# Performance work log

Measured on AMD Instinct MI355X. Metric: run time of the kernel, lower is better.

## Reference

```python
import jax, jax.numpy as jnp
import numpy as np

MAX_NODES = 8192
MAX_EDGES = 16384
D = 64
NEG = -1e10


def setup_inputs() -> dict:
    key = jax.random.key(0)
    k1, k2, k3, k4, k5, k6 = jax.random.split(key, 6)
    N, E = MAX_NODES, MAX_EDGES
    nodes = jax.random.normal(k1, (N, D), jnp.float32)
    edges = jax.random.normal(k2, (E, D), jnp.float32)
    receivers = jax.random.randint(k3, (E,), 0, N, jnp.int32)
    senders = jax.random.randint(k4, (E,), 0, N, jnp.int32)
    active_nodes = jnp.ones((N,), jnp.float32)
    active_edges = (jnp.arange(E) < E // 4).astype(jnp.float32)  # prefix of active edges
    Wq = jax.random.normal(k5, (D, D), jnp.float32) / jnp.sqrt(jnp.float32(D))
    Wp = jax.random.normal(k6, (D, 1), jnp.float32) * 0.05
    bq = jnp.zeros((D,), jnp.float32)
    bp = jnp.full((1,), -4.0, jnp.float32)
    return dict(nodes=nodes, edges=edges, receivers=receivers, senders=senders,
                active_nodes=active_nodes, active_edges=active_edges,
                Wq=Wq, bq=bq, Wp=Wp, bp=bp)


def _incr_edges(aedges, n):
    # Closed form of n steps of x <- clip(x @ (I + superdiag), 0, 1):
    # out[j] = 1 iff any(aedges[j-n : j+1]) != 0, then last slot forced to 0.
    c = jnp.cumsum(aedges)
    idx = jnp.arange(aedges.shape[0])
    prev = jnp.where(idx - n - 1 >= 0, c[jnp.clip(idx - n - 1, 0)], 0.0)
    out = ((c - prev) > 0).astype(aedges.dtype)
    return out.at[-1].set(0.0)


def reference(nodes, edges, receivers, senders, active_nodes, active_edges, Wq, bq, Wp, bp):
    N, E = MAX_NODES, MAX_EDGES
    key = jax.random.key(42)
    key_prob, key_edges, key_samp = jax.random.split(key, 3)
    nids = jnp.arange(N)
    e_active = active_edges.sum().astype(jnp.int32)

    # 1-2. edge-generation probability per node + Bernoulli sampling of generators
    probs = jax.nn.sigmoid(nodes @ Wp + bp)[:, 0]                       # [N]
    gens = (jax.random.uniform(key_prob, (N,)) < probs * active_nodes).astype(jnp.float32)

    # 3-4. queries and pairwise cosine-similarity scores[i, j] = cos(q_i, h_j)
    queries = nodes @ Wq + bq                                           # [N, D]
    num = queries @ nodes.T                                             # [N, N]
    qn = jnp.sum(queries * queries, -1)                                 # [N]
    hn = jnp.sum(nodes * nodes, -1)                                     # [N]
    scores = num / (jnp.sqrt(qn[:, None] * hn[None, :]) + 1e-8)
    scores = jnp.clip(scores, -10000.0, 10000.0)
    scores = jnp.where(active_nodes[None, :] > 0, scores, NEG)
    gens = gens * (scores.max(-1) > -jnp.inf).astype(jnp.float32)       # threshold = -inf
    scores = jnp.where(jnp.eye(N, dtype=bool), NEG, scores)             # no self-loops

    # 5. sample target j* per generating node (softmax mode)
    select = jnp.where(gens > 0, jax.random.categorical(key_samp, scores, axis=-1), 0)

    # drop generators whose edge (i, j*) already exists
    is_s = nids[:, None] == senders[None, :]                            # [N, E]
    is_r = select[:, None] == receivers[None, :]                        # [N, E]
    exist = jnp.logical_and(is_s, is_r).any(-1) & (gens > 0)
    gens = jnp.where(exist, 0.0, gens)

    # 6. scatter new edges into the fixed-size buffers
    allowed = E - e_active - 1
    n_gens = jnp.clip(gens.astype(jnp.int32).sum(), 0, allowed)
    naedges = _incr_edges(active_edges, n_gens)
    mask_new = naedges * (1.0 - active_edges)                           # [E]
    new_edges = edges + jax.random.normal(key_edges, edges.shape) * mask_new[:, None]

    t1 = (jnp.cumsum(gens) * gens - 1.0).astype(jnp.int32) + (e_active * gens).astype(jnp.int32)
    nsend = jax.ops.segment_sum(nids, t1, E)
    nsend = jnp.where(mask_new > 0, nsend, senders)

    t2 = jnp.cumsum(gens) * gens - gens
    t2 = jnp.where(gens > 0, t2.astype(jnp.int32), -1) + (e_active * gens).astype(jnp.int32)
    nrec = jax.ops.segment_sum(select, t2, E)
    nrec = jnp.where(mask_new > 0, nrec, receivers)

    nrec = jnp.where(naedges > 0, nrec, N - 1)
    nsend = jnp.where(naedges > 0, nsend, N - 1)
    return new_edges, nsend, nrec, naedges
```

## Files before the change

kernel.cpp:

```cpp
#include <hip/hip_runtime.h>
#include <stdint.h>

#define NN 8192
#define NE 16384
#define DD 64
#define GCAP 512
#define SLICES 32
#define NEGV -1e10f
#define TINYF 1.17549435e-38f
#define SQRT2F 1.41421356237f

__device__ __forceinline__ uint2 tf2x32(uint32_t k0, uint32_t k1, uint32_t x0, uint32_t x1) {
  uint32_t ks2 = k0 ^ k1 ^ 0x1BD11BDAu;
  x0 += k0; x1 += k1;
#define TF_R(r) { x0 += x1; x1 = (x1 << (r)) | (x1 >> (32 - (r))); x1 ^= x0; }
  TF_R(13) TF_R(15) TF_R(26) TF_R(6)
  x0 += k1; x1 += ks2 + 1u;
  TF_R(17) TF_R(29) TF_R(16) TF_R(24)
  x0 += ks2; x1 += k0 + 2u;
  TF_R(13) TF_R(15) TF_R(26) TF_R(6)
  x0 += k0; x1 += k1 + 3u;
  TF_R(17) TF_R(29) TF_R(16) TF_R(24)
  x0 += k1; x1 += ks2 + 4u;
  TF_R(13) TF_R(15) TF_R(26) TF_R(6)
  x0 += ks2; x1 += k0 + 5u;
#undef TF_R
  return make_uint2(x0, x1);
}
__device__ __forceinline__ uint2 jax_subkey(uint32_t i) { return tf2x32(0u, 42u, 0u, i); }
__device__ __forceinline__ uint32_t rbits(uint2 k, uint32_t idx) {
  uint2 r = tf2x32(k.x, k.y, 0u, idx);
  return r.x ^ r.y;
}
__device__ __forceinline__ float u01f(uint32_t b) {
  return __uint_as_float((b >> 9) | 0x3F800000u) - 1.0f;
}
__device__ __forceinline__ float erfinv_xla(float x) {
  float w = -log1pf(-x * x);
  float p;
  if (w < 5.0f) {
    w -= 2.5f;
    p = 2.81022636e-08f;
    p = fmaf(p, w, 3.43273939e-07f);
    p = fmaf(p, w, -3.5233877e-06f);
    p = fmaf(p, w, -4.39150654e-06f);
    p = fmaf(p, w, 0.00021858087f);
    p = fmaf(p, w, -0.00125372503f);
    p = fmaf(p, w, -0.00417768164f);
    p = fmaf(p, w, 0.246640727f);
    p = fmaf(p, w, 1.50140941f);
  } else {
    w = sqrtf(w) - 3.0f;
    p = -0.000200214257f;
    p = fmaf(p, w, 0.000100950558f);
    p = fmaf(p, w, 0.00134934322f);
    p = fmaf(p, w, -0.00367342844f);
    p = fmaf(p, w, 0.00573950773f);
    p = fmaf(p, w, -0.0076224613f);
    p = fmaf(p, w, 0.00943887047f);
    p = fmaf(p, w, 1.00167406f);
    p = fmaf(p, w, 2.83297682f);
  }
  return p * x;
}
__device__ __forceinline__ float jax_normal(uint2 k, uint32_t idx) {
  float f = u01f(rbits(k, idx));
  float lo = __uint_as_float(0xBF7FFFFFu);
  float u = fmaxf(lo, f * 2.0f + lo);
  return SQRT2F * erfinv_xla(u);
}
__device__ __forceinline__ float jax_gumbel(uint2 k, uint32_t idx) {
  float f = u01f(rbits(k, idx));
  float u = fmaxf(TINYF, f + TINYF);
  return -logf(-logf(u));
}


__global__ void sg_gens(const float* __restrict__ nodes, const float* __restrict__ Wp,
                        const float* __restrict__ bp, const float* __restrict__ anodes,
                        int* __restrict__ gens0, float* __restrict__ hn) {
  int lane = threadIdx.x & 63;
  int i = blockIdx.x * 4 + (threadIdx.x >> 6);
  float v = nodes[i * DD + lane];
  float ss = v * v;
  float dp = v * Wp[lane];
  for (int off = 32; off > 0; off >>= 1) {
    ss += __shfl_xor(ss, off, 64);
    dp += __shfl_xor(dp, off, 64);
  }
  if (lane == 0) {
    hn[i] = ss;
    float x = dp + bp[0];
    float p = 1.0f / (1.0f + expf(-x));
    uint2 kp = jax_subkey(0u);
    float u = u01f(rbits(kp, (uint32_t)i));
    gens0[i] = (u < p * anodes[i]) ? 1 : 0;
  }
}

__global__ void sg_scan(const float* __restrict__ aedges, const int* __restrict__ gens0,
                        int* __restrict__ c, int* __restrict__ gidx, int* __restrict__ sc) {
  __shared__ int ts[256];
  int t = threadIdx.x;
  int base = t * 64;
  uint64_t bits = 0;
  int s = 0;
  const float4* a4 = (const float4*)(aedges + base);
  for (int k4 = 0; k4 < 16; k4++) {
    float4 v = a4[k4];
    if (v.x != 0.0f) { bits |= 1ull << (4 * k4 + 0); s++; }
    if (v.y != 0.0f) { bits |= 1ull << (4 * k4 + 1); s++; }
    if (v.z != 0.0f) { bits |= 1ull << (4 * k4 + 2); s++; }
    if (v.w != 0.0f) { bits |= 1ull << (4 * k4 + 3); s++; }
  }
  ts[t] = s;
  __syncthreads();
  for (int off = 1; off < 256; off <<= 1) {
    int add = (t >= off) ? ts[t - off] : 0;
    __syncthreads();
    ts[t] += add;
    __syncthreads();
  }
  int run = ts[t] - s;
  for (int k = 0; k < 64; k++) {
    run += (int)((bits >> k) & 1ull);
    c[base + k] = run;
  }
  if (t == 255) { sc[1] = ts[255]; sc[2] = NE - ts[255] - 1; }
  __syncthreads();
  int b2 = t * 32;
  uint32_t gb = 0;
  int s2 = 0;
  const int4* g4 = (const int4*)(gens0 + b2);
  for (int k4 = 0; k4 < 8; k4++) {
    int4 v = g4[k4];
    if (v.x) { gb |= 1u << (4 * k4 + 0); s2++; }
    if (v.y) { gb |= 1u << (4 * k4 + 1); s2++; }
    if (v.z) { gb |= 1u << (4 * k4 + 2); s2++; }
    if (v.w) { gb |= 1u << (4 * k4 + 3); s2++; }
  }
  ts[t] = s2;
  __syncthreads();
  for (int off = 1; off < 256; off <<= 1) {
    int add = (t >= off) ? ts[t - off] : 0;
    __syncthreads();
    ts[t] += add;
    __syncthreads();
  }
  int r = ts[t] - s2;
  for (int k = 0; k < 32; k++)
    if ((gb >> k) & 1u) gidx[r++] = b2 + k;
  if (t == 255) sc[0] = ts[255];
}

__global__ void sg_query(const float* __restrict__ nodes, const float* __restrict__ Wq,
                         const float* __restrict__ bq, const int* __restrict__ gidx,
                         const int* __restrict__ sc, float* __restrict__ qg,
                         float* __restrict__ qnrm) {
  int g = blockIdx.x;
  int G = min(sc[0], GCAP);
  if (g >= G) return;
  int i = gidx[g];
  int t = threadIdx.x;
  const float* nr = nodes + (size_t)i * DD;
  float acc = bq[t];
  for (int k = 0; k < DD; k++) acc = fmaf(nr[k], Wq[k * DD + t], acc);
  qg[g * DD + t] = acc;
  float ss = acc * acc;
  for (int off = 32; off > 0; off >>= 1) ss += __shfl_xor(ss, off, 64);
  if (t == 0) qnrm[g] = ss;
}

__global__ __launch_bounds__(256) void sg_part(
    const float* __restrict__ nodes, const float* __restrict__ anodes,
    const float* __restrict__ hn, const int* __restrict__ gidx,
    const int* __restrict__ sc, const float* __restrict__ qg,
    const float* __restrict__ qnrm, float* __restrict__ party,
    int* __restrict__ partj) {
  __shared__ float sq[4][DD];
  __shared__ float sqn[4];
  __shared__ int si[4];
  __shared__ float wy[4][4];
  __shared__ int wj[4][4];
  int G = min(sc[0], GCAP);
  int nGq = (G + 3) >> 2;
  int total = nGq * SLICES;
  int t = threadIdx.x;
  int wid = t >> 6, lane = t & 63;
  uint2 ks = jax_subkey(2u);
  for (int item = blockIdx.x; item < total; item += gridDim.x) {
    int gq = item >> 5, s = item & 31;
    int g0 = gq * 4;
    if (t < DD) {
      for (int u = 0; u < 4; u++)
        sq[u][t] = (g0 + u < G) ? qg[(g0 + u) * DD + t] : 0.0f;
    }
    if (t < 4) {
      int g = g0 + t;
      si[t] = (g < G) ? gidx[g] : -1;
      sqn[t] = (g < G) ? qnrm[g] : 1.0f;
    }
    __syncthreads();
    int j = s * 256 + t;
    float4 nv[16];
    const float4* np4 = (const float4*)(nodes + (size_t)j * DD);
    for (int k4 = 0; k4 < 16; k4++) nv[k4] = np4[k4];
    float hnj = hn[j];
    float act = anodes[j];
    float yy[4];
    for (int u = 0; u < 4; u++) {
      int iu = si[u];
      if (iu < 0) { yy[u] = -INFINITY; continue; }
      float num = 0.0f;
      for (int k4 = 0; k4 < 16; k4++) {
        const float4 qv = *(const float4*)&sq[u][4 * k4];
        num += nv[k4].x * qv.x + nv[k4].y * qv.y + nv[k4].z * qv.z + nv[k4].w * qv.w;
      }
      float denom = sqrtf(sqn[u] * hnj) + 1e-8f;
      float sco = num / denom;
      sco = fminf(fmaxf(sco, -10000.0f), 10000.0f);
      if (!(act > 0.0f)) sco = NEGV;
      if (j == iu) sco = NEGV;
      yy[u] = sco + jax_gumbel(ks, (uint32_t)iu * (uint32_t)NN + (uint32_t)j);
    }
    for (int u = 0; u < 4; u++) {
      float y = yy[u];
      int bj = j;
      for (int off = 32; off > 0; off >>= 1) {
        float oy = __shfl_xor(y, off, 64);
        int oj = __shfl_xor(bj, off, 64);
        if (oy > y || (oy == y && oj < bj)) { y = oy; bj = oj; }
      }
      if (lane == 0) { wy[u][wid] = y; wj[u][wid] = bj; }
    }
    __syncthreads();
    if (t < 4) {
      int u = t;
      if (g0 + u < G) {
        float y = wy[u][0];
        int bj = wj[u][0];
        for (int w = 1; w < 4; w++) {
          if (wy[u][w] > y || (wy[u][w] == y && wj[u][w] < bj)) { y = wy[u][w]; bj = wj[u][w]; }
        }
        party[(g0 + u) * SLICES + s] = y;
        partj[(g0 + u) * SLICES + s] = bj;
      }
    }
    __syncthreads();
  }
}

__global__ void sg_reduce(const int* __restrict__ sc, const float* __restrict__ party,
                          const int* __restrict__ partj, int* __restrict__ sel,
                          int* __restrict__ keptf) {
  int g = blockIdx.x;
  int G = min(sc[0], GCAP);
  if (g >= G) return;
  int t = threadIdx.x;
  float y = (t < SLICES) ? party[g * SLICES + t] : -INFINITY;
  int bj = (t < SLICES) ? partj[g * SLICES + t] : 0x7fffffff;
  for (int off = 32; off > 0; off >>= 1) {
    float oy = __shfl_xor(y, off, 64);
    int oj = __shfl_xor(bj, off, 64);
    if (oy > y || (oy == y && oj < bj)) { y = oy; bj = oj; }
  }
  if (t == 0) { sel[g] = bj; keptf[g] = 1; }
}

__global__ void sg_exist2(const int* __restrict__ senders, const int* __restrict__ receivers,
                          const int* __restrict__ gidx, const int* __restrict__ sel,
                          const int* __restrict__ sc, int* __restrict__ keptf) {
  __shared__ int lg[GCAP], ls[GCAP];
  int G = min(sc[0], GCAP);
  int t = threadIdx.x;
  for (int g = t; g < G; g += 256) { lg[g] = gidx[g]; ls[g] = sel[g]; }
  __syncthreads();
  int e = blockIdx.x * 256 + t;
  int se = senders[e], re = receivers[e];
  for (int g = 0; g < G; g++)
    if (se == lg[g] && re == ls[g]) keptf[g] = 0;
}

__global__ void sg_rank(const int* __restrict__ gidx, const int* __restrict__ sel,
                        const int* __restrict__ keptf, int* __restrict__ sc,
                        int* __restrict__ fid, int* __restrict__ fsel) {
  __shared__ int ts[256];
  int t = threadIdx.x;
  int G = min(sc[0], GCAP);
  int base = t * 32;
  int s = 0;
  for (int k = 0; k < 32; k++) { int g = base + k; if (g < G) s += keptf[g]; }
  ts[t] = s;
  __syncthreads();
  for (int off = 1; off < 256; off <<= 1) {
    int add = (t >= off) ? ts[t - off] : 0;
    __syncthreads();
    ts[t] += add;
    __syncthreads();
  }
  int r = ts[t] - s;
  for (int k = 0; k < 32; k++) {
    int g = base + k;
    if (g < G && keptf[g]) { fid[r] = gidx[g]; fsel[r] = sel[g]; r++; }
  }
  if (t == 255) {
    int kt = ts[255];
    int allowed = sc[2];
    int ng = kt > 0 ? kt : 0;
    if (ng > allowed) ng = allowed;
    sc[3] = kt; sc[4] = ng;
  }
}

__global__ void sg_mask(const float* __restrict__ aedges, const int* __restrict__ senders,
                        const int* __restrict__ receivers, const int* __restrict__ c,
                        const int* __restrict__ sc, const int* __restrict__ fid,
                        const int* __restrict__ fsel, float* __restrict__ out_send,
                        float* __restrict__ out_rec, float* __restrict__ out_na) {
  int e = blockIdx.x * 256 + threadIdx.x;
  if (e >= NE) return;
  int n = sc[4], ea = sc[1], kept = sc[3];
  int ce = c[e];
  int pidx = e - n - 1;
  int prev = (pidx >= 0) ? c[pidx] : 0;
  int na = ((ce - prev) > 0) ? 1 : 0;
  if (e == NE - 1) na = 0;
  float a = aedges[e];
  float mv = na ? (1.0f - a) : 0.0f;
  float ns, nr;
  if (!na) {
    ns = nr = (float)(NN - 1);
  } else if (mv > 0.0f) {
    int r = e - ea;
    bool ok = (r >= 0 && r < kept);
    ns = ok ? (float)fid[r] : 0.0f;
    nr = ok ? (float)fsel[r] : 0.0f;
  } else {
    ns = (float)senders[e];
    nr = (float)receivers[e];
  }
  out_send[e] = ns;
  out_rec[e] = nr;
  out_na[e] = (float)na;
}

__global__ void sg_edges(const float* __restrict__ edges, const float* __restrict__ aedges,
                         const int* __restrict__ c, const int* __restrict__ sc,
                         float* __restrict__ out_edges) {
  int t4 = blockIdx.x * 256 + threadIdx.x;
  float4 v = ((const float4*)edges)[t4];
  int e = t4 >> 4;
  int n = sc[4];
  int ce = c[e];
  int pidx = e - n - 1;
  int prev = (pidx >= 0) ? c[pidx] : 0;
  int na = ((ce - prev) > 0 && e != NE - 1) ? 1 : 0;
  float mv = na ? (1.0f - aedges[e]) : 0.0f;
  if (mv != 0.0f) {
    uint2 ke = jax_subkey(1u);
    uint32_t base = (uint32_t)t4 * 4u;
    v.x += jax_normal(ke, base + 0u) * mv;
    v.y += jax_normal(ke, base + 1u) * mv;
    v.z += jax_normal(ke, base + 2u) * mv;
    v.w += jax_normal(ke, base + 3u) * mv;
  }
  ((float4*)out_edges)[t4] = v;
}

extern "C" void kernel_launch(void* const* d_in, const int* in_sizes, int n_in,
                              void* d_out, int out_size, void* d_ws, size_t ws_size,
                              hipStream_t stream) {
  const float* nodes     = (const float*)d_in[0];
  const float* edges     = (const float*)d_in[1];
  const int*   receivers = (const int*)d_in[2];
  const int*   senders   = (const int*)d_in[3];
  const float* anodes    = (const float*)d_in[4];
  const float* aedges    = (const float*)d_in[5];
  const float* Wq        = (const float*)d_in[6];
  const float* bq        = (const float*)d_in[7];
  const float* Wp        = (const float*)d_in[8];
  const float* bp        = (const float*)d_in[9];

  float* out       = (float*)d_out;
  float* out_edges = out;
  float* out_send  = out + (size_t)NE * DD;
  float* out_rec   = out_send + NE;
  float* out_na    = out_rec + NE;

  int* sc     = (int*)d_ws;
  int* gens0  = sc + 8;
  int* gidx   = gens0 + NN;
  int* sel    = gidx + NN;
  int* keptf  = sel + GCAP;
  int* fid    = keptf + GCAP;
  int* fsel   = fid + GCAP;
  int* c      = fsel + GCAP;
  int* partj  = c + NE;
  float* hn   = (float*)(partj + GCAP * SLICES);
  float* qg   = hn + NN;
  float* qnrm = qg + GCAP * DD;
  float* party= qnrm + GCAP;

  sg_gens   <<<NN / 4, 256, 0, stream>>>(nodes, Wp, bp, anodes, gens0, hn);
  sg_scan   <<<1, 256, 0, stream>>>(aedges, gens0, c, gidx, sc);
  sg_query  <<<GCAP, 64, 0, stream>>>(nodes, Wq, bq, gidx, sc, qg, qnrm);
  sg_part   <<<4096, 256, 0, stream>>>(nodes, anodes, hn, gidx, sc, qg, qnrm, party, partj);
  sg_reduce <<<GCAP, 64, 0, stream>>>(sc, party, partj, sel, keptf);
  sg_exist2 <<<NE / 256, 256, 0, stream>>>(senders, receivers, gidx, sel, sc, keptf);
  sg_rank   <<<1, 256, 0, stream>>>(gidx, sel, keptf, sc, fid, fsel);
  sg_mask   <<<NE / 256, 256, 0, stream>>>(aedges, senders, receivers, c, sc, fid, fsel,
                                           out_send, out_rec, out_na);
  sg_edges  <<<NE * DD / 4 / 256, 256, 0, stream>>>(edges, aedges, c, sc, out_edges);
}
```

Before: 142.3 us.

## Fuse query projection, selection reduce, existence check and output kernels

```diff
diff --git a/kernel.cpp b/kernel.cpp
--- a/kernel.cpp
+++ b/kernel.cpp
@@ -153,29 +153,11 @@
   if (t == 255) sc[0] = ts[255];
 }
 
-__global__ void sg_query(const float* __restrict__ nodes, const float* __restrict__ Wq,
-                         const float* __restrict__ bq, const int* __restrict__ gidx,
-                         const int* __restrict__ sc, float* __restrict__ qg,
-                         float* __restrict__ qnrm) {
-  int g = blockIdx.x;
-  int G = min(sc[0], GCAP);
-  if (g >= G) return;
-  int i = gidx[g];
-  int t = threadIdx.x;
-  const float* nr = nodes + (size_t)i * DD;
-  float acc = bq[t];
-  for (int k = 0; k < DD; k++) acc = fmaf(nr[k], Wq[k * DD + t], acc);
-  qg[g * DD + t] = acc;
-  float ss = acc * acc;
-  for (int off = 32; off > 0; off >>= 1) ss += __shfl_xor(ss, off, 64);
-  if (t == 0) qnrm[g] = ss;
-}
-
 __global__ __launch_bounds__(256) void sg_part(
     const float* __restrict__ nodes, const float* __restrict__ anodes,
     const float* __restrict__ hn, const int* __restrict__ gidx,
-    const int* __restrict__ sc, const float* __restrict__ qg,
-    const float* __restrict__ qnrm, float* __restrict__ party,
+    const int* __restrict__ sc, const float* __restrict__ Wq,
+    const float* __restrict__ bq, float* __restrict__ party,
     int* __restrict__ partj) {
   __shared__ float sq[4][DD];
   __shared__ float sqn[4];
@@ -191,14 +173,31 @@
   for (int item = blockIdx.x; item < total; item += gridDim.x) {
     int gq = item >> 5, s = item & 31;
     int g0 = gq * 4;
+    __syncthreads();
+    if (t < 4) { int g = g0 + t; si[t] = (g < G) ? gidx[g] : -1; }
+    __syncthreads();
     if (t < DD) {
-      for (int u = 0; u < 4; u++)
-        sq[u][t] = (g0 + u < G) ? qg[(g0 + u) * DD + t] : 0.0f;
-    }
-    if (t < 4) {
-      int g = g0 + t;
-      si[t] = (g < G) ? gidx[g] : -1;
-      sqn[t] = (g < G) ? qnrm[g] : 1.0f;
+      int i0 = si[0] < 0 ? 0 : si[0];
+      int i1 = si[1] < 0 ? 0 : si[1];
+      int i2 = si[2] < 0 ? 0 : si[2];
+      int i3 = si[3] < 0 ? 0 : si[3];
+      float a0 = bq[t], a1 = a0, a2 = a0, a3 = a0;
+      for (int k = 0; k < DD; k++) {
+        float w = Wq[k * DD + t];
+        a0 = fmaf(nodes[i0 * DD + k], w, a0);
+        a1 = fmaf(nodes[i1 * DD + k], w, a1);
+        a2 = fmaf(nodes[i2 * DD + k], w, a2);
+        a3 = fmaf(nodes[i3 * DD + k], w, a3);
+      }
+      sq[0][t] = a0; sq[1][t] = a1; sq[2][t] = a2; sq[3][t] = a3;
+      float s0 = a0 * a0, s1 = a1 * a1, s2 = a2 * a2, s3 = a3 * a3;
+      for (int off = 32; off > 0; off >>= 1) {
+        s0 += __shfl_xor(s0, off, 64);
+        s1 += __shfl_xor(s1, off, 64);
+        s2 += __shfl_xor(s2, off, 64);
+        s3 += __shfl_xor(s3, off, 64);
+      }
+      if (t == 0) { sqn[0] = s0; sqn[1] = s1; sqn[2] = s2; sqn[3] = s3; }
     }
     __syncthreads();
     int j = s * 256 + t;
@@ -246,39 +245,37 @@
         partj[(g0 + u) * SLICES + s] = bj;
       }
     }
-    __syncthreads();
-  }
-}
-
-__global__ void sg_reduce(const int* __restrict__ sc, const float* __restrict__ party,
-                          const int* __restrict__ partj, int* __restrict__ sel,
-                          int* __restrict__ keptf) {
+  }
+}
+
+__global__ void sg_sel(const int* __restrict__ sc, const float* __restrict__ party,
+                       const int* __restrict__ partj, const int* __restrict__ gidx,
+                       const int* __restrict__ senders, const int* __restrict__ receivers,
+                       int* __restrict__ sel, int* __restrict__ keptf) {
   int g = blockIdx.x;
   int G = min(sc[0], GCAP);
   if (g >= G) return;
   int t = threadIdx.x;
-  float y = (t < SLICES) ? party[g * SLICES + t] : -INFINITY;
-  int bj = (t < SLICES) ? partj[g * SLICES + t] : 0x7fffffff;
-  for (int off = 32; off > 0; off >>= 1) {
-    float oy = __shfl_xor(y, off, 64);
-    int oj = __shfl_xor(bj, off, 64);
-    if (oy > y || (oy == y && oj < bj)) { y = oy; bj = oj; }
-  }
-  if (t == 0) { sel[g] = bj; keptf[g] = 1; }
-}
-
-__global__ void sg_exist2(const int* __restrict__ senders, const int* __restrict__ receivers,
-                          const int* __restrict__ gidx, const int* __restrict__ sel,
-                          const int* __restrict__ sc, int* __restrict__ keptf) {
-  __shared__ int lg[GCAP], ls[GCAP];
-  int G = min(sc[0], GCAP);
-  int t = threadIdx.x;
-  for (int g = t; g < G; g += 256) { lg[g] = gidx[g]; ls[g] = sel[g]; }
-  __syncthreads();
-  int e = blockIdx.x * 256 + t;
-  int se = senders[e], re = receivers[e];
-  for (int g = 0; g < G; g++)
-    if (se == lg[g] && re == ls[g]) keptf[g] = 0;
+  __shared__ int js_s;
+  __shared__ int ex;
+  if (t < 64) {
+    float y = (t < SLICES) ? party[g * SLICES + t] : -INFINITY;
+    int bj = (t < SLICES) ? partj[g * SLICES + t] : 0x7fffffff;
+    for (int off = 32; off > 0; off >>= 1) {
+      float oy = __shfl_xor(y, off, 64);
+      int oj = __shfl_xor(bj, off, 64);
+      if (oy > y || (oy == y && oj < bj)) { y = oy; bj = oj; }
+    }
+    if (t == 0) { js_s = bj; ex = 0; }
+  }
+  __syncthreads();
+  int i = gidx[g], js = js_s;
+  int f = 0;
+  for (int e = t; e < NE; e += 256)
+    f |= (senders[e] == i && receivers[e] == js) ? 1 : 0;
+  if (f) ex = 1;
+  __syncthreads();
+  if (t == 0) { sel[g] = js; keptf[g] = ex ? 0 : 1; }
 }
 
 __global__ void sg_rank(const int* __restrict__ gidx, const int* __restrict__ sel,
@@ -312,41 +309,12 @@
   }
 }
 
-__global__ void sg_mask(const float* __restrict__ aedges, const int* __restrict__ senders,
-                        const int* __restrict__ receivers, const int* __restrict__ c,
-                        const int* __restrict__ sc, const int* __restrict__ fid,
-                        const int* __restrict__ fsel, float* __restrict__ out_send,
-                        float* __restrict__ out_rec, float* __restrict__ out_na) {
-  int e = blockIdx.x * 256 + threadIdx.x;
-  if (e >= NE) return;
-  int n = sc[4], ea = sc[1], kept = sc[3];
-  int ce = c[e];
-  int pidx = e - n - 1;
-  int prev = (pidx >= 0) ? c[pidx] : 0;
-  int na = ((ce - prev) > 0) ? 1 : 0;
-  if (e == NE - 1) na = 0;
-  float a = aedges[e];
-  float mv = na ? (1.0f - a) : 0.0f;
-  float ns, nr;
-  if (!na) {
-    ns = nr = (float)(NN - 1);
-  } else if (mv > 0.0f) {
-    int r = e - ea;
-    bool ok = (r >= 0 && r < kept);
-    ns = ok ? (float)fid[r] : 0.0f;
-    nr = ok ? (float)fsel[r] : 0.0f;
-  } else {
-    ns = (float)senders[e];
-    nr = (float)receivers[e];
-  }
-  out_send[e] = ns;
-  out_rec[e] = nr;
-  out_na[e] = (float)na;
-}
-
-__global__ void sg_edges(const float* __restrict__ edges, const float* __restrict__ aedges,
+__global__ void sg_write(const float* __restrict__ edges, const float* __restrict__ aedges,
+                         const int* __restrict__ senders, const int* __restrict__ receivers,
                          const int* __restrict__ c, const int* __restrict__ sc,
-                         float* __restrict__ out_edges) {
+                         const int* __restrict__ fid, const int* __restrict__ fsel,
+                         float* __restrict__ out_edges, float* __restrict__ out_send,
+                         float* __restrict__ out_rec, float* __restrict__ out_na) {
   int t4 = blockIdx.x * 256 + threadIdx.x;
   float4 v = ((const float4*)edges)[t4];
   int e = t4 >> 4;
@@ -358,13 +326,31 @@
   float mv = na ? (1.0f - aedges[e]) : 0.0f;
   if (mv != 0.0f) {
     uint2 ke = jax_subkey(1u);
-    uint32_t base = (uint32_t)t4 * 4u;
-    v.x += jax_normal(ke, base + 0u) * mv;
-    v.y += jax_normal(ke, base + 1u) * mv;
-    v.z += jax_normal(ke, base + 2u) * mv;
-    v.w += jax_normal(ke, base + 3u) * mv;
+    uint32_t b = (uint32_t)t4 * 4u;
+    v.x += jax_normal(ke, b + 0u) * mv;
+    v.y += jax_normal(ke, b + 1u) * mv;
+    v.z += jax_normal(ke, b + 2u) * mv;
+    v.w += jax_normal(ke, b + 3u) * mv;
   }
   ((float4*)out_edges)[t4] = v;
+  if ((t4 & 15) == 0) {
+    int ea = sc[1], kept = sc[3];
+    float ns, nr;
+    if (!na) {
+      ns = nr = (float)(NN - 1);
+    } else if (mv > 0.0f) {
+      int r = e - ea;
+      bool ok = (r >= 0 && r < kept);
+      ns = ok ? (float)fid[r] : 0.0f;
+      nr = ok ? (float)fsel[r] : 0.0f;
+    } else {
+      ns = (float)senders[e];
+      nr = (float)receivers[e];
+    }
+    out_send[e] = ns;
+    out_rec[e] = nr;
+    out_na[e] = (float)na;
+  }
 }
 
 extern "C" void kernel_launch(void* const* d_in, const int* in_sizes, int n_in,
@@ -397,18 +383,14 @@
   int* c      = fsel + GCAP;
   int* partj  = c + NE;
   float* hn   = (float*)(partj + GCAP * SLICES);
-  float* qg   = hn + NN;
-  float* qnrm = qg + GCAP * DD;
-  float* party= qnrm + GCAP;
-
-  sg_gens   <<<NN / 4, 256, 0, stream>>>(nodes, Wp, bp, anodes, gens0, hn);
-  sg_scan   <<<1, 256, 0, stream>>>(aedges, gens0, c, gidx, sc);
-  sg_query  <<<GCAP, 64, 0, stream>>>(nodes, Wq, bq, gidx, sc, qg, qnrm);
-  sg_part   <<<4096, 256, 0, stream>>>(nodes, anodes, hn, gidx, sc, qg, qnrm, party, partj);
-  sg_reduce <<<GCAP, 64, 0, stream>>>(sc, party, partj, sel, keptf);
-  sg_exist2 <<<NE / 256, 256, 0, stream>>>(senders, receivers, gidx, sel, sc, keptf);
-  sg_rank   <<<1, 256, 0, stream>>>(gidx, sel, keptf, sc, fid, fsel);
-  sg_mask   <<<NE / 256, 256, 0, stream>>>(aedges, senders, receivers, c, sc, fid, fsel,
-                                           out_send, out_rec, out_na);
-  sg_edges  <<<NE * DD / 4 / 256, 256, 0, stream>>>(edges, aedges, c, sc, out_edges);
-}
+  float* party= hn + NN;
+
+  sg_gens  <<<NN / 4, 256, 0, stream>>>(nodes, Wp, bp, anodes, gens0, hn);
+  sg_scan  <<<1, 256, 0, stream>>>(aedges, gens0, c, gidx, sc);
+  sg_part  <<<2048, 256, 0, stream>>>(nodes, anodes, hn, gidx, sc, Wq, bq, party, partj);
+  sg_sel   <<<GCAP, 256, 0, stream>>>(sc, party, partj, gidx, senders, receivers, sel, keptf);
+  sg_rank  <<<1, 256, 0, stream>>>(gidx, sel, keptf, sc, fid, fsel);
+  sg_write <<<NE * DD / 4 / 256, 256, 0, stream>>>(edges, aedges, senders, receivers, c, sc,
+                                                   fid, fsel, out_edges, out_send, out_rec,
+                                                   out_na);
+}
```

Result: slower. 150.8 us (+6.0%).
